# Performance work log

Measured on AMD Instinct MI355X. Metric: run time of the kernel, lower is better.

Reference implementation:

```python
import jax, jax.numpy as jnp
import numpy as np

H = 16  # n_heads (matches init_kwargs)


def setup_inputs() -> dict:
    key = jax.random.key(0)
    ks = jax.random.split(key, 11)
    B, L, D = 4, 2048, 1024
    inp = {
        "query": jax.random.normal(ks[0], (B, L, D), jnp.float32),
        "key": jax.random.normal(ks[1], (B, L, D), jnp.float32),
        "value": jax.random.normal(ks[2], (B, L, D), jnp.float32),
        "mask": jnp.ones((1, L, L), jnp.int32),
        "Wq": jax.random.normal(ks[3], (D, D), jnp.float32) / np.sqrt(D).astype(np.float32),
        "bq": jax.random.normal(ks[4], (D,), jnp.float32) * 0.02,
        "Wk": jax.random.normal(ks[5], (D, D), jnp.float32) / np.sqrt(D).astype(np.float32),
        "bk": jax.random.normal(ks[6], (D,), jnp.float32) * 0.02,
        "Wv": jax.random.normal(ks[7], (D, D), jnp.float32) / np.sqrt(D).astype(np.float32),
        "bv": jax.random.normal(ks[8], (D,), jnp.float32) * 0.02,
        "Wo": jax.random.normal(ks[9], (D, D), jnp.float32) / np.sqrt(D).astype(np.float32),
        "bo": jax.random.normal(ks[10], (D,), jnp.float32) * 0.02,
    }
    return inp


def reference(query, key, value, mask, Wq, bq, Wk, bk, Wv, bv, Wo, bo):
    B, L, D = query.shape
    dk = D // H
    scale = float(dk) ** -0.5

    def proj(x, W, b):
        # torch Linear: x @ W.T + b, then split heads -> (B, H, L, dk)
        return (x @ W.T + b).reshape(B, -1, H, dk).transpose(0, 2, 1, 3)

    q = proj(query, Wq, bq)
    k = proj(key, Wk, bk)
    v = proj(value, Wv, bv)

    scores = jnp.einsum('bhqd,bhkd->bhqk', q, k) * scale  # (B,H,L,L)
    # mask unsqueezed over head dim; masked_fill(mask == 0, -1e9)
    scores = jnp.where(mask[:, None, :, :] == 0, jnp.float32(-1e9), scores)
    p_attn = jax.nn.softmax(scores, axis=-1)  # dropout omitted (eval mode)
    x = jnp.einsum('bhqk,bhkd->bhqd', p_attn, v)
    x = x.transpose(0, 2, 1, 3).reshape(B, -1, D)
    return x @ Wo.T + bo
```

## Files before the change

### kernel.cpp

```cpp
#include <hip/hip_runtime.h>
#include <hip/hip_bf16.h>
#include <type_traits>


typedef __hip_bfloat16 bf16;
typedef __attribute__((ext_vector_type(8))) short s8;
typedef __attribute__((ext_vector_type(4))) short s4;
typedef __attribute__((ext_vector_type(4))) float f4;

constexpr int Bb = 4, Ls = 2048, Dd = 1024, Hh = 16, DK = 64;
constexpr int BHn = Bb * Hh;
constexpr int Mrows = Bb * Ls;

typedef const __attribute__((address_space(1))) unsigned int* gas_t;
typedef __attribute__((address_space(3))) unsigned int* las_t;
__device__ __forceinline__ void dma16(const void* g, void* l) {
    __builtin_amdgcn_global_load_lds((gas_t)g, (las_t)l, 16, 0, 0);
}

__device__ __forceinline__ s8 ld8(const float* __restrict__ p) {
    const float4 a = *(const float4*)p;
    const float4 b = *(const float4*)(p + 4);
    union { bf16 h[8]; s8 v; } u;
    u.h[0] = __float2bfloat16(a.x); u.h[1] = __float2bfloat16(a.y);
    u.h[2] = __float2bfloat16(a.z); u.h[3] = __float2bfloat16(a.w);
    u.h[4] = __float2bfloat16(b.x); u.h[5] = __float2bfloat16(b.y);
    u.h[6] = __float2bfloat16(b.z); u.h[7] = __float2bfloat16(b.w);
    return u.v;
}
__device__ __forceinline__ void st1(bf16* p, float v)  { *p = __float2bfloat16(v); }
__device__ __forceinline__ void st1(float* p, float v) { *p = v; }

__global__ __launch_bounds__(256) void conv_bf16(
    const float* __restrict__ in, bf16* __restrict__ out, int n8)
{
    const int i = blockIdx.x * 256 + threadIdx.x;
    if (i < n8) *(s8*)&out[(size_t)i * 8] = ld8(in + (size_t)i * 8);
}

template<int MODE, typename WT, typename OT>
__global__ __launch_bounds__(256) void gemm_nt(
    const bf16* __restrict__ A, const WT* __restrict__ W,
    const float* __restrict__ bias, OT* __restrict__ out,
    int M, int N, int K, float osc)
{
    __shared__ __align__(16) bf16 lA[128 * 32];
    __shared__ __align__(16) bf16 lB[128 * 32];
    const int tid  = threadIdx.x;
    const int wave = tid >> 6, lane = tid & 63;
    const int qd = lane >> 4, lr = lane & 15;
    const int wm = (wave & 1) * 64, wn = (wave >> 1) * 64;
    const int row0 = blockIdx.x * 128, col0 = blockIdx.y * 128;

    f4 acc[4][4] = {};

    const int c0 = tid, c1 = tid + 256;
    const int wr0 = c0 >> 2, wk0 = (c0 & 3) * 8;
    const int wr1 = c1 >> 2, wk1 = (c1 & 3) * 8;

    for (int kt = 0; kt < K; kt += 32) {
#pragma unroll
        for (int r = 0; r < 2; r++) {
            const int s = r * 256 + tid;
            const int row = s >> 2, c = s & 3;
            dma16(A + (size_t)(row0 + row) * K + kt + c * 8, &lA[s * 8]);
        }
        if constexpr (std::is_same<WT, bf16>::value) {
#pragma unroll
            for (int r = 0; r < 2; r++) {
                const int s = r * 256 + tid;
                const int row = s >> 2, c = s & 3;
                dma16(W + (size_t)(col0 + row) * K + kt + c * 8, &lB[s * 8]);
            }
        } else {
            *(s8*)&lB[c0 * 8] = ld8(W + (size_t)(col0 + wr0) * K + kt + wk0);
            *(s8*)&lB[c1 * 8] = ld8(W + (size_t)(col0 + wr1) * K + kt + wk1);
        }
        __syncthreads();
        s8 af[4], bfm[4];
#pragma unroll
        for (int i = 0; i < 4; i++) af[i]  = *(const s8*)&lA[(wm + i * 16 + lr) * 32 + qd * 8];
#pragma unroll
        for (int j = 0; j < 4; j++) bfm[j] = *(const s8*)&lB[(wn + j * 16 + lr) * 32 + qd * 8];
#pragma unroll
        for (int i = 0; i < 4; i++)
#pragma unroll
            for (int j = 0; j < 4; j++)
                acc[i][j] = __builtin_amdgcn_mfma_f32_16x16x32_bf16(af[i], bfm[j], acc[i][j], 0, 0, 0);
        __syncthreads();
    }

#pragma unroll
    for (int j = 0; j < 4; j++) {
        const int colg = col0 + wn + j * 16 + lr;
        const float bv = bias[colg];
#pragma unroll
        for (int i = 0; i < 4; i++) {
            const int rowb = row0 + wm + i * 16 + qd * 4;
            if (MODE == 2) {
                const int b = rowb >> 11, l = rowb & (Ls - 1);
                const int h = colg >> 6, d = colg & (DK - 1);
                union { bf16 h4[4]; s4 v; } u;
#pragma unroll
                for (int ri = 0; ri < 4; ri++)
                    u.h4[ri] = __float2bfloat16((acc[i][j][ri] + bv) * osc);
                *(s4*)&((bf16*)out)[(((size_t)(b * Hh + h) * DK) + d) * Ls + l] = u.v;
            } else {
#pragma unroll
                for (int ri = 0; ri < 4; ri++) {
                    const int rowg = rowb + ri;
                    const float v = (acc[i][j][ri] + bv) * osc;
                    size_t idx;
                    if (MODE == 0) {
                        idx = (size_t)rowg * N + colg;
                    } else {
                        const int b = rowg >> 11, l = rowg & (Ls - 1);
                        const int h = colg >> 6, d = colg & (DK - 1);
                        idx = (((size_t)(b * Hh + h) * Ls) + l) * DK + d;
                    }
                    st1(&out[idx], v);
                }
            }
        }
    }
}

__global__ __launch_bounds__(256) void pack_mask(
    const int* __restrict__ m, unsigned long long* __restrict__ bits)
{
    const int g = blockIdx.x * 256 + threadIdx.x;
    const unsigned long long b = __ballot(m[g] != 0);
    if ((threadIdx.x & 63) == 0) bits[g >> 6] = b;
}

__global__ __launch_bounds__(512, 2) void attn(
    const bf16* __restrict__ Q, const bf16* __restrict__ K,
    const bf16* __restrict__ Vt, const unsigned long long* __restrict__ mbits,
    bf16* __restrict__ X)
{
    __shared__ __align__(16) bf16 lK[2][64 * 64];
    __shared__ __align__(16) bf16 lV[2][64 * 64];

    const int blk = blockIdx.x;
    const int bh = blk >> 4;
    const int q0 = (blk & 15) * 128;
    const int tid = threadIdx.x;
    const int wave = tid >> 6, lane = tid & 63;
    const int qd = lane >> 4, lr = lane & 15;
    const int qw0 = q0 + wave * 16;

    const bf16* Qb = Q  + (size_t)bh * Ls * DK;
    const bf16* Kb = K  + (size_t)bh * Ls * DK;
    const bf16* Vb = Vt + (size_t)bh * DK * Ls;

    const s8 bq0 = *(const s8*)(Qb + (size_t)(qw0 + lr) * DK + qd * 8);
    const s8 bq1 = *(const s8*)(Qb + (size_t)(qw0 + lr) * DK + 32 + qd * 8);

    f4 o[4] = {};
    float lp = 0.f;

    const int srow = tid >> 3, scs = tid & 7;
    const int sc = scs ^ ((srow & 3) | ((srow >> 1) & 4));
    const bf16* gK = Kb + (size_t)srow * DK + sc * 8;
    const bf16* gV = Vb + (size_t)srow * Ls + sc * 8;

    const size_t mrow = (size_t)(qw0 + lr) * (Ls / 64);

    dma16(gK, &lK[0][tid * 8]);
    dma16(gV, &lV[0][tid * 8]);
    unsigned long long wcur = mbits[mrow];
    __syncthreads();

    int cur = 0;
    for (int kt = 0; kt < Ls / 64; ++kt) {
        unsigned long long wnext = 0;
        if (kt + 1 < Ls / 64) {
            const int nb = cur ^ 1;
            dma16(gK + (size_t)(kt + 1) * 64 * DK, &lK[nb][tid * 8]);
            dma16(gV + (size_t)(kt + 1) * 64,      &lV[nb][tid * 8]);
            wnext = mbits[mrow + kt + 1];
        }

        f4 st[4];
        __builtin_amdgcn_s_setprio(1);
#pragma unroll
        for (int mt = 0; mt < 4; mt++) {
            const int rk = 32 * (mt >> 1) + 8 * (lr >> 2) + 4 * (mt & 1) + (lr & 3);
            const int fr = (rk & 3) | ((rk >> 1) & 4);
            const s8 ak0 = *(const s8*)&lK[cur][(rk * 8 + ((qd)     ^ fr)) * 8];
            const s8 ak1 = *(const s8*)&lK[cur][(rk * 8 + ((4 + qd) ^ fr)) * 8];
            f4 z = {};
            z = __builtin_amdgcn_mfma_f32_16x16x32_bf16(ak0, bq0, z, 0, 0, 0);
            z = __builtin_amdgcn_mfma_f32_16x16x32_bf16(ak1, bq1, z, 0, 0, 0);
            st[mt] = z;
        }
        __builtin_amdgcn_s_setprio(0);

        if (__ballot(wcur == ~0ULL) != ~0ULL) {
#pragma unroll
            for (int mt = 0; mt < 4; mt++)
#pragma unroll
                for (int ri = 0; ri < 4; ri++) {
                    const int kbit = 32 * (mt >> 1) + 8 * qd + 4 * (mt & 1) + ri;
                    if (!((wcur >> kbit) & 1ULL)) st[mt][ri] = -1e9f;
                }
        }

        unsigned pk[4][2];
#pragma unroll
        for (int mt = 0; mt < 4; mt++) {
#pragma unroll
            for (int u = 0; u < 2; u++) {
                const float p0 = __builtin_amdgcn_exp2f(st[mt][2 * u]);
                const float p1 = __builtin_amdgcn_exp2f(st[mt][2 * u + 1]);
                lp += p0 + p1;
                unsigned r;
                asm("v_cvt_pk_bf16_f32 %0, %1, %2" : "=v"(r) : "v"(p0), "v"(p1));
                pk[mt][u] = r;
            }
        }

#pragma unroll
        for (int h = 0; h < 2; h++) {
            union { unsigned u[4]; s8 v; } bp;
            bp.u[0] = pk[2 * h][0];
            bp.u[1] = pk[2 * h][1];
            bp.u[2] = pk[2 * h + 1][0];
            bp.u[3] = pk[2 * h + 1][1];
            __builtin_amdgcn_s_setprio(1);
#pragma unroll
            for (int dt = 0; dt < 4; dt++) {
                const int rowd = dt * 16 + lr;
                const int fv = (rowd & 3) | ((rowd >> 1) & 4);
                const s8 av = *(const s8*)&lV[cur][(rowd * 8 + ((h * 4 + qd) ^ fv)) * 8];
                o[dt] = __builtin_amdgcn_mfma_f32_16x16x32_bf16(av, bp.v, o[dt], 0, 0, 0);
            }
            __builtin_amdgcn_s_setprio(0);
        }

        __syncthreads();
        cur ^= 1;
        wcur = wnext;
    }

    float lsum = lp;
    lsum += __shfl_xor(lsum, 16, 64);
    lsum += __shfl_xor(lsum, 32, 64);
    const int b = bh >> 4, head = bh & 15;
    const float inv = 1.f / lsum;
    const int qrow = qw0 + lr;
#pragma unroll
    for (int dt = 0; dt < 4; dt++) {
        union { bf16 h4[4]; s4 v; } u;
#pragma unroll
        for (int ri = 0; ri < 4; ri++)
            u.h4[ri] = __float2bfloat16(o[dt][ri] * inv);
        *(s4*)&X[((size_t)(b * Ls + qrow)) * Dd + head * 64 + dt * 16 + qd * 4] = u.v;
    }
}

extern "C" void kernel_launch(void* const* d_in, const int* in_sizes, int n_in,
                              void* d_out, int out_size, void* d_ws, size_t ws_size,
                              hipStream_t stream) {
    const float* q_in = (const float*)d_in[0];
    const float* k_in = (const float*)d_in[1];
    const float* v_in = (const float*)d_in[2];
    const int*   mask = (const int*)d_in[3];
    const float* Wq = (const float*)d_in[4];  const float* bq = (const float*)d_in[5];
    const float* Wk = (const float*)d_in[6];  const float* bk = (const float*)d_in[7];
    const float* Wv = (const float*)d_in[8];  const float* bv = (const float*)d_in[9];
    const float* Wo = (const float*)d_in[10]; const float* bo = (const float*)d_in[11];
    float* out = (float*)d_out;

    char* ws = (char*)d_ws;
    const size_t sz = (size_t)BHn * Ls * DK * sizeof(bf16);
    bf16* S0 = (bf16*)(ws);
    bf16* S1 = (bf16*)(ws + sz);
    bf16* S2 = (bf16*)(ws + 2 * sz);
    bf16* S3 = (bf16*)(ws + 3 * sz);
    unsigned long long* mb = (unsigned long long*)(ws + 4 * sz);
    const int NW = Dd * Dd;

    dim3 gg(Mrows / 128, Dd / 128);
    const int gA = (Mrows * Dd / 8 + 255) / 256;
    const int gW = (NW / 8 + 255) / 256;

    const float QSC = 0.125f * 1.44269504f;

    conv_bf16<<<gA, 256, 0, stream>>>(v_in, S0, Mrows * Dd / 8);
    conv_bf16<<<gW, 256, 0, stream>>>(Wv, S1, NW / 8);
    gemm_nt<2, bf16, bf16><<<gg, 256, 0, stream>>>(S0, S1, bv, S3, Mrows, Dd, Dd, 1.0f);

    conv_bf16<<<gA, 256, 0, stream>>>(k_in, S0, Mrows * Dd / 8);
    conv_bf16<<<gW, 256, 0, stream>>>(Wk, S1 + NW, NW / 8);
    gemm_nt<1, bf16, bf16><<<gg, 256, 0, stream>>>(S0, S1 + NW, bk, S2, Mrows, Dd, Dd, 1.0f);

    conv_bf16<<<gA, 256, 0, stream>>>(q_in, S0, Mrows * Dd / 8);
    gemm_nt<1, float, bf16><<<gg, 256, 0, stream>>>(S0, Wq, bq, S1, Mrows, Dd, Dd, QSC);

    pack_mask<<<(Ls * Ls) / 256, 256, 0, stream>>>(mask, mb);
    attn<<<BHn * (Ls / 128), 512, 0, stream>>>(S1, S2, S3, mb, S0);

    conv_bf16<<<gW, 256, 0, stream>>>(Wo, S2, NW / 8);
    gemm_nt<0, bf16, float><<<gg, 256, 0, stream>>>(S0, S2, bo, out, Mrows, Dd, Dd, 1.0f);
}
```

Baseline: 416.4 us.

## Double-buffer GEMM LDS tiles with K=64 steps and XOR-swizzled layout

Rewrites the projection GEMM main loop to use two LDS buffers, prefetching the next K tile while MFMAs run on the current one. The K tile grows from 32 to 64, and an XOR swizzle on the 16-byte chunk index is meant to avoid LDS bank conflicts on fragment reads. One barrier per iteration replaces two. LDS use grows to 64KB per block, which may lower occupancy. The fp32-weight path still uses synchronous loads.

```diff
diff --git a/kernel.cpp b/kernel.cpp
--- a/kernel.cpp
+++ b/kernel.cpp
@@ -31,6 +31,8 @@
 __device__ __forceinline__ void st1(bf16* p, float v)  { *p = __float2bfloat16(v); }
 __device__ __forceinline__ void st1(float* p, float v) { *p = v; }
 
+__device__ __forceinline__ int fswz(int r) { return (r & 3) | ((r >> 1) & 4); }
+
 __global__ __launch_bounds__(256) void conv_bf16(
     const float* __restrict__ in, bf16* __restrict__ out, int n8)
 {
@@ -44,8 +46,8 @@
     const float* __restrict__ bias, OT* __restrict__ out,
     int M, int N, int K, float osc)
 {
-    __shared__ __align__(16) bf16 lA[128 * 32];
-    __shared__ __align__(16) bf16 lB[128 * 32];
+    __shared__ __align__(16) bf16 lA[2][128 * 64];
+    __shared__ __align__(16) bf16 lB[2][128 * 64];
     const int tid  = threadIdx.x;
     const int wave = tid >> 6, lane = tid & 63;
     const int qd = lane >> 4, lr = lane & 15;
@@ -54,40 +56,75 @@
 
     f4 acc[4][4] = {};
 
-    const int c0 = tid, c1 = tid + 256;
-    const int wr0 = c0 >> 2, wk0 = (c0 & 3) * 8;
-    const int wr1 = c1 >> 2, wk1 = (c1 & 3) * 8;
-
-    for (int kt = 0; kt < K; kt += 32) {
-#pragma unroll
-        for (int r = 0; r < 2; r++) {
+    const int NT = K >> 6;
+
+    {
+#pragma unroll
+        for (int r = 0; r < 4; r++) {
             const int s = r * 256 + tid;
-            const int row = s >> 2, c = s & 3;
-            dma16(A + (size_t)(row0 + row) * K + kt + c * 8, &lA[s * 8]);
-        }
-        if constexpr (std::is_same<WT, bf16>::value) {
-#pragma unroll
-            for (int r = 0; r < 2; r++) {
+            const int row = s >> 3;
+            const int c = (s & 7) ^ fswz(row);
+            dma16(A + (size_t)(row0 + row) * K + c * 8, &lA[0][s * 8]);
+        }
+#pragma unroll
+        for (int r = 0; r < 4; r++) {
+            const int s = r * 256 + tid;
+            const int row = s >> 3;
+            const int c = (s & 7) ^ fswz(row);
+            if constexpr (std::is_same<WT, bf16>::value)
+                dma16(W + (size_t)(col0 + row) * K + c * 8, &lB[0][s * 8]);
+            else
+                *(s8*)&lB[0][s * 8] = ld8(W + (size_t)(col0 + row) * K + c * 8);
+        }
+    }
+    __syncthreads();
+
+    int cur = 0;
+    for (int t = 0; t < NT; ++t) {
+        if (t + 1 < NT) {
+            const int nb = cur ^ 1;
+            const int kt = (t + 1) * 64;
+#pragma unroll
+            for (int r = 0; r < 4; r++) {
                 const int s = r * 256 + tid;
-                const int row = s >> 2, c = s & 3;
-                dma16(W + (size_t)(col0 + row) * K + kt + c * 8, &lB[s * 8]);
-            }
-        } else {
-            *(s8*)&lB[c0 * 8] = ld8(W + (size_t)(col0 + wr0) * K + kt + wk0);
-            *(s8*)&lB[c1 * 8] = ld8(W + (size_t)(col0 + wr1) * K + kt + wk1);
-        }
+                const int row = s >> 3;
+                const int c = (s & 7) ^ fswz(row);
+                dma16(A + (size_t)(row0 + row) * K + kt + c * 8, &lA[nb][s * 8]);
+            }
+#pragma unroll
+            for (int r = 0; r < 4; r++) {
+                const int s = r * 256 + tid;
+                const int row = s >> 3;
+                const int c = (s & 7) ^ fswz(row);
+                if constexpr (std::is_same<WT, bf16>::value)
+                    dma16(W + (size_t)(col0 + row) * K + kt + c * 8, &lB[nb][s * 8]);
+                else
+                    *(s8*)&lB[nb][s * 8] = ld8(W + (size_t)(col0 + row) * K + kt + c * 8);
+            }
+        }
+
+#pragma unroll
+        for (int kk = 0; kk < 2; kk++) {
+            s8 af[4], bfm[4];
+#pragma unroll
+            for (int i = 0; i < 4; i++) {
+                const int row = wm + i * 16 + lr;
+                af[i] = *(const s8*)&lA[cur][(row * 8 + ((kk * 4 + qd) ^ fswz(row))) * 8];
+            }
+#pragma unroll
+            for (int j = 0; j < 4; j++) {
+                const int row = wn + j * 16 + lr;
+                bfm[j] = *(const s8*)&lB[cur][(row * 8 + ((kk * 4 + qd) ^ fswz(row))) * 8];
+            }
+#pragma unroll
+            for (int i = 0; i < 4; i++)
+#pragma unroll
+                for (int j = 0; j < 4; j++)
+                    acc[i][j] = __builtin_amdgcn_mfma_f32_16x16x32_bf16(af[i], bfm[j], acc[i][j], 0, 0, 0);
+        }
+
         __syncthreads();
-        s8 af[4], bfm[4];
-#pragma unroll
-        for (int i = 0; i < 4; i++) af[i]  = *(const s8*)&lA[(wm + i * 16 + lr) * 32 + qd * 8];
-#pragma unroll
-        for (int j = 0; j < 4; j++) bfm[j] = *(const s8*)&lB[(wn + j * 16 + lr) * 32 + qd * 8];
-#pragma unroll
-        for (int i = 0; i < 4; i++)
-#pragma unroll
-            for (int j = 0; j < 4; j++)
-                acc[i][j] = __builtin_amdgcn_mfma_f32_16x16x32_bf16(af[i], bfm[j], acc[i][j], 0, 0, 0);
-        __syncthreads();
+        cur ^= 1;
     }
 
 #pragma unroll
```

Result: faster. 381.8 us (-8.3%).

## Fuse fp32-to-bf16 activation conversion into GEMMs and double-buffer swizzled LDS tiles

Applied to the files above, without the earlier changes.

The three activation conversion kernels are removed: the projection GEMMs now load fp32 activations directly and convert them to bf16 while staging into LDS. The GEMM is restructured to 512 threads with a K-tile of 64, double-buffered LDS with a single barrier per iteration, and an XOR swizzle on LDS chunk indices to reduce bank conflicts. This removes three full-size activation round trips through global memory and the extra launches. In exchange, fp32 register-path loads can't use async LDS DMA, and per-wave accumulator tiles shrink to 64x32.

```diff
diff --git a/kernel.cpp b/kernel.cpp
--- a/kernel.cpp
+++ b/kernel.cpp
@@ -31,6 +31,8 @@
 __device__ __forceinline__ void st1(bf16* p, float v)  { *p = __float2bfloat16(v); }
 __device__ __forceinline__ void st1(float* p, float v) { *p = v; }
 
+__device__ __forceinline__ int fswz(int r) { return (r & 3) | ((r >> 1) & 4); }
+
 __global__ __launch_bounds__(256) void conv_bf16(
     const float* __restrict__ in, bf16* __restrict__ out, int n8)
 {
@@ -38,60 +40,80 @@
     if (i < n8) *(s8*)&out[(size_t)i * 8] = ld8(in + (size_t)i * 8);
 }
 
-template<int MODE, typename WT, typename OT>
-__global__ __launch_bounds__(256) void gemm_nt(
-    const bf16* __restrict__ A, const WT* __restrict__ W,
+template<int MODE, typename AT, typename WT, typename OT>
+__global__ __launch_bounds__(512, 2) void gemm_nt(
+    const AT* __restrict__ A, const WT* __restrict__ W,
     const float* __restrict__ bias, OT* __restrict__ out,
     int M, int N, int K, float osc)
 {
-    __shared__ __align__(16) bf16 lA[128 * 32];
-    __shared__ __align__(16) bf16 lB[128 * 32];
+    __shared__ __align__(16) bf16 lA[2][128 * 64];
+    __shared__ __align__(16) bf16 lB[2][128 * 64];
     const int tid  = threadIdx.x;
     const int wave = tid >> 6, lane = tid & 63;
     const int qd = lane >> 4, lr = lane & 15;
-    const int wm = (wave & 1) * 64, wn = (wave >> 1) * 64;
+    const int wm = (wave & 1) * 64, wn = (wave >> 1) * 32;
     const int row0 = blockIdx.x * 128, col0 = blockIdx.y * 128;
 
-    f4 acc[4][4] = {};
-
-    const int c0 = tid, c1 = tid + 256;
-    const int wr0 = c0 >> 2, wk0 = (c0 & 3) * 8;
-    const int wr1 = c1 >> 2, wk1 = (c1 & 3) * 8;
-
-    for (int kt = 0; kt < K; kt += 32) {
-#pragma unroll
-        for (int r = 0; r < 2; r++) {
-            const int s = r * 256 + tid;
-            const int row = s >> 2, c = s & 3;
-            dma16(A + (size_t)(row0 + row) * K + kt + c * 8, &lA[s * 8]);
-        }
-        if constexpr (std::is_same<WT, bf16>::value) {
-#pragma unroll
-            for (int r = 0; r < 2; r++) {
-                const int s = r * 256 + tid;
-                const int row = s >> 2, c = s & 3;
-                dma16(W + (size_t)(col0 + row) * K + kt + c * 8, &lB[s * 8]);
-            }
-        } else {
-            *(s8*)&lB[c0 * 8] = ld8(W + (size_t)(col0 + wr0) * K + kt + wk0);
-            *(s8*)&lB[c1 * 8] = ld8(W + (size_t)(col0 + wr1) * K + kt + wk1);
-        }
+    f4 acc[4][2] = {};
+
+    const int NT = K >> 6;
+
+    const int s0 = tid, s1 = tid + 512;
+    const int r0 = s0 >> 3, c0 = (s0 & 7) ^ fswz(r0);
+    const int r1 = s1 >> 3, c1 = (s1 & 7) ^ fswz(r1);
+
+#define STAGE(buf, kt)                                                          \
+    {                                                                           \
+        if constexpr (std::is_same<AT, bf16>::value) {                          \
+            dma16(A + (size_t)(row0 + r0) * K + (kt) + c0 * 8, &lA[buf][s0 * 8]); \
+            dma16(A + (size_t)(row0 + r1) * K + (kt) + c1 * 8, &lA[buf][s1 * 8]); \
+        } else {                                                                \
+            *(s8*)&lA[buf][s0 * 8] = ld8(A + (size_t)(row0 + r0) * K + (kt) + c0 * 8); \
+            *(s8*)&lA[buf][s1 * 8] = ld8(A + (size_t)(row0 + r1) * K + (kt) + c1 * 8); \
+        }                                                                       \
+        if constexpr (std::is_same<WT, bf16>::value) {                          \
+            dma16(W + (size_t)(col0 + r0) * K + (kt) + c0 * 8, &lB[buf][s0 * 8]); \
+            dma16(W + (size_t)(col0 + r1) * K + (kt) + c1 * 8, &lB[buf][s1 * 8]); \
+        } else {                                                                \
+            *(s8*)&lB[buf][s0 * 8] = ld8(W + (size_t)(col0 + r0) * K + (kt) + c0 * 8); \
+            *(s8*)&lB[buf][s1 * 8] = ld8(W + (size_t)(col0 + r1) * K + (kt) + c1 * 8); \
+        }                                                                       \
+    }
+
+    STAGE(0, 0);
+    __syncthreads();
+
+    int cur = 0;
+    for (int t = 0; t < NT; ++t) {
+        if (t + 1 < NT) { STAGE(cur ^ 1, (t + 1) * 64); }
+
+#pragma unroll
+        for (int kk = 0; kk < 2; kk++) {
+            s8 af[4], bfm[2];
+#pragma unroll
+            for (int i = 0; i < 4; i++) {
+                const int row = wm + i * 16 + lr;
+                af[i] = *(const s8*)&lA[cur][(row * 8 + ((kk * 4 + qd) ^ fswz(row))) * 8];
+            }
+#pragma unroll
+            for (int j = 0; j < 2; j++) {
+                const int row = wn + j * 16 + lr;
+                bfm[j] = *(const s8*)&lB[cur][(row * 8 + ((kk * 4 + qd) ^ fswz(row))) * 8];
+            }
+#pragma unroll
+            for (int i = 0; i < 4; i++)
+#pragma unroll
+                for (int j = 0; j < 2; j++)
+                    acc[i][j] = __builtin_amdgcn_mfma_f32_16x16x32_bf16(af[i], bfm[j], acc[i][j], 0, 0, 0);
+        }
+
         __syncthreads();
-        s8 af[4], bfm[4];
-#pragma unroll
-        for (int i = 0; i < 4; i++) af[i]  = *(const s8*)&lA[(wm + i * 16 + lr) * 32 + qd * 8];
-#pragma unroll
-        for (int j = 0; j < 4; j++) bfm[j] = *(const s8*)&lB[(wn + j * 16 + lr) * 32 + qd * 8];
-#pragma unroll
-        for (int i = 0; i < 4; i++)
-#pragma unroll
-            for (int j = 0; j < 4; j++)
-                acc[i][j] = __builtin_amdgcn_mfma_f32_16x16x32_bf16(af[i], bfm[j], acc[i][j], 0, 0, 0);
-        __syncthreads();
-    }
-
-#pragma unroll
-    for (int j = 0; j < 4; j++) {
+        cur ^= 1;
+    }
+#undef STAGE
+
+#pragma unroll
+    for (int j = 0; j < 2; j++) {
         const int colg = col0 + wn + j * 16 + lr;
         const float bv = bias[colg];
 #pragma unroll
@@ -282,25 +304,21 @@
     const int NW = Dd * Dd;
 
     dim3 gg(Mrows / 128, Dd / 128);
-    const int gA = (Mrows * Dd / 8 + 255) / 256;
     const int gW = (NW / 8 + 255) / 256;
 
     const float QSC = 0.125f * 1.44269504f;
 
-    conv_bf16<<<gA, 256, 0, stream>>>(v_in, S0, Mrows * Dd / 8);
     conv_bf16<<<gW, 256, 0, stream>>>(Wv, S1, NW / 8);
-    gemm_nt<2, bf16, bf16><<<gg, 256, 0, stream>>>(S0, S1, bv, S3, Mrows, Dd, Dd, 1.0f);
-
-    conv_bf16<<<gA, 256, 0, stream>>>(k_in, S0, Mrows * Dd / 8);
+    gemm_nt<2, float, bf16, bf16><<<gg, 512, 0, stream>>>(v_in, S1, bv, S3, Mrows, Dd, Dd, 1.0f);
+
     conv_bf16<<<gW, 256, 0, stream>>>(Wk, S1 + NW, NW / 8);
-    gemm_nt<1, bf16, bf16><<<gg, 256, 0, stream>>>(S0, S1 + NW, bk, S2, Mrows, Dd, Dd, 1.0f);
-
-    conv_bf16<<<gA, 256, 0, stream>>>(q_in, S0, Mrows * Dd / 8);
-    gemm_nt<1, float, bf16><<<gg, 256, 0, stream>>>(S0, Wq, bq, S1, Mrows, Dd, Dd, QSC);
+    gemm_nt<1, float, bf16, bf16><<<gg, 512, 0, stream>>>(k_in, S1 + NW, bk, S2, Mrows, Dd, Dd, 1.0f);
+
+    gemm_nt<1, float, float, bf16><<<gg, 512, 0, stream>>>(q_in, Wq, bq, S1, Mrows, Dd, Dd, QSC);
 
     pack_mask<<<(Ls * Ls) / 256, 256, 0, stream>>>(mask, mb);
     attn<<<BHn * (Ls / 128), 512, 0, stream>>>(S1, S2, S3, mb, S0);
 
     conv_bf16<<<gW, 256, 0, stream>>>(Wo, S2, NW / 8);
-    gemm_nt<0, bf16, float><<<gg, 256, 0, stream>>>(S0, S2, bo, out, Mrows, Dd, Dd, 1.0f);
-}
+    gemm_nt<0, bf16, bf16, float><<<gg, 512, 0, stream>>>(S0, S2, bo, out, Mrows, Dd, Dd, 1.0f);
+}
```

Result: faster. 383.7 us (-7.8%).
